# Kernel tuning notes

Hardware: AMD Instinct MI355X
Metric: run time of the kernel (lower is better)

The kernel has to match this reference:

```python
import jax, jax.numpy as jnp
import numpy as np

EPS = 1e-6
FEAT = 1024
HEADS = 16
HDIM = FEAT // HEADS
FF = 500


def setup_inputs() -> dict:
    key = jax.random.key(0)
    ks = jax.random.split(key, 12)
    B, S = 4, 2048
    inp = {
        "x": jax.random.normal(ks[0], (B, S, FEAT), jnp.float32),
        "mask": jax.random.randint(ks[1], (B, S, S), 0, 2, jnp.int32),
        "alpha1": jnp.ones((FEAT,), jnp.float32),
        "bias1": jnp.zeros((FEAT,), jnp.float32),
        "alpha2": jnp.ones((FEAT,), jnp.float32),
        "bias2": jnp.zeros((FEAT,), jnp.float32),
        "Wq": jax.random.normal(ks[2], (FEAT, FEAT), jnp.float32) * (1.0 / np.sqrt(FEAT)),
        "bq": jnp.zeros((FEAT,), jnp.float32),
        "Wk": jax.random.normal(ks[3], (FEAT, FEAT), jnp.float32) * (1.0 / np.sqrt(FEAT)),
        "bk": jnp.zeros((FEAT,), jnp.float32),
        "Wv": jax.random.normal(ks[4], (FEAT, FEAT), jnp.float32) * (1.0 / np.sqrt(FEAT)),
        "bv": jnp.zeros((FEAT,), jnp.float32),
        "Wo": jax.random.normal(ks[5], (FEAT, FEAT), jnp.float32) * (1.0 / np.sqrt(FEAT)),
        "bo": jnp.zeros((FEAT,), jnp.float32),
        "W1": jax.random.normal(ks[6], (FEAT, FF), jnp.float32) * (1.0 / np.sqrt(FEAT)),
        "b1": jnp.zeros((FF,), jnp.float32),
        "W2": jax.random.normal(ks[7], (FF, FEAT), jnp.float32) * (1.0 / np.sqrt(FF)),
        "b2": jnp.zeros((FEAT,), jnp.float32),
    }
    return inp


def _norm(x, alpha, bias):
    m = jnp.mean(x, axis=-1, keepdims=True)
    # torch.std uses Bessel's correction (ddof=1)
    s = jnp.std(x, axis=-1, keepdims=True, ddof=1)
    return alpha * (x - m) / (s + EPS) + bias


def _attn(x2, mask, Wq, bq, Wk, bk, Wv, bv, Wo, bo):
    B, S, _ = x2.shape
    q = (x2 @ Wq + bq).reshape(B, S, HEADS, HDIM)
    k = (x2 @ Wk + bk).reshape(B, S, HEADS, HDIM)
    v = (x2 @ Wv + bv).reshape(B, S, HEADS, HDIM)
    scores = jnp.einsum("bqhd,bkhd->bhqk", q, k) / np.sqrt(HDIM).astype(np.float32)
    # faithful to source: masked positions filled with -1e-09 (not -1e9)
    scores = jnp.where(mask[:, None, :, :] == 0, jnp.float32(-1e-09), scores)
    probs = jax.nn.softmax(scores, axis=-1)
    out = jnp.einsum("bhqk,bkhd->bqhd", probs, v).reshape(B, S, FEAT)
    return out @ Wo + bo


def reference(x, mask, alpha1, bias1, alpha2, bias2, Wq, bq, Wk, bk, Wv, bv, Wo, bo, W1, b1, W2, b2):
    x2 = _norm(x, alpha1, bias1)
    x = x + _attn(x2, mask, Wq, bq, Wk, bk, Wv, bv, Wo, bo)
    x2 = _norm(x, alpha2, bias2)
    h = jax.nn.elu(x2 @ W1 + b1)
    x = x + (h @ W2 + b2)
    return x
```

## Files before the change

kernel.cpp:

```cpp
#include <hip/hip_runtime.h>
#include <hip/hip_bf16.h>
#include <math.h>

#define BATCH 4
#define SEQ 2048
#define FEAT 1024
#define HEADS 16
#define HDIM 64
#define FF 500
#define FFP 512
#define ROWS (BATCH * SEQ)
#define QKVSTR 3072

typedef unsigned short ushortT;
typedef __attribute__((ext_vector_type(8))) short short8;
typedef __attribute__((ext_vector_type(4))) float floatx4;

#if defined(__has_builtin) && __has_builtin(__builtin_amdgcn_exp2f)
#define EXP2F(x) __builtin_amdgcn_exp2f(x)
#else
#define EXP2F(x) exp2f(x)
#endif

__device__ __forceinline__ unsigned short f2bf(float f) {
    unsigned int u = __builtin_bit_cast(unsigned int, f);
    u += 0x7fffu + ((u >> 16) & 1u);
    return (unsigned short)(u >> 16);
}
__device__ __forceinline__ float bf2f(short b) {
    unsigned int u = ((unsigned int)(unsigned short)b) << 16;
    return __builtin_bit_cast(float, u);
}

__device__ __forceinline__ void async16(void* lds, const void* g) {
    __builtin_amdgcn_global_load_lds(
        (const __attribute__((address_space(1))) unsigned int*)g,
        (__attribute__((address_space(3))) unsigned int*)lds, 16, 0, 0);
}

__global__ void wt_kernel(const float* __restrict__ W, ushortT* __restrict__ Wt,
                          int K, int N, int Kp)
{
    __shared__ float T[64][65];
    const int n0 = blockIdx.x * 64, k0 = blockIdx.y * 64;
    const int tid = threadIdx.x;
    const int r = tid >> 4;
    const int c = (tid & 15) * 4;
    #pragma unroll
    for (int i = 0; i < 4; i++) {
        const int kk = k0 + r + i * 16;
        #pragma unroll
        for (int e = 0; e < 4; e++) {
            const int nn = n0 + c + e;
            T[r + i * 16][c + e] = (kk < K && nn < N) ? W[(size_t)kk * N + nn] : 0.0f;
        }
    }
    __syncthreads();
    #pragma unroll
    for (int i = 0; i < 4; i++) {
        const int nn = r + i * 16;
        ushort4 o;
        o.x = f2bf(T[c + 0][nn]);
        o.y = f2bf(T[c + 1][nn]);
        o.z = f2bf(T[c + 2][nn]);
        o.w = f2bf(T[c + 3][nn]);
        *(ushort4*)(Wt + (size_t)(n0 + nn) * Kp + k0 + c) = o;
    }
}

__global__ void pad_bias_kernel(const float* __restrict__ b, float* __restrict__ bp)
{
    const int i = threadIdx.x;
    if (i < FFP) bp[i] = (i < FF) ? b[i] : 0.0f;
}

__global__ void concat_bias_kernel(const float* __restrict__ bq, const float* __restrict__ bk,
                                   const float* __restrict__ bv, float* __restrict__ o)
{
    const int i = blockIdx.x * 256 + threadIdx.x;
    o[i] = (i < 1024) ? bq[i] : ((i < 2048) ? bk[i - 1024] : bv[i - 2048]);
}

__global__ void maskbits_kernel(const int* __restrict__ mask,
                                unsigned int* __restrict__ bits)
{
    const size_t g = (size_t)blockIdx.x * 256 + threadIdx.x;
    const int lane = threadIdx.x & 63;
    const unsigned long long bal = __ballot(mask[g] != 0);
    if (lane == 0)  bits[g >> 5] = (unsigned int)bal;
    if (lane == 32) bits[g >> 5] = (unsigned int)(bal >> 32);
}

__global__ void ln_kernel(const float* __restrict__ x,
                          const float* __restrict__ alpha,
                          const float* __restrict__ bias,
                          ushortT* __restrict__ out)
{
    __shared__ float red[256];
    const int row = blockIdx.x;
    const int tid = threadIdx.x;
    float4 v = ((const float4*)(x + (size_t)row * FEAT))[tid];

    red[tid] = v.x + v.y + v.z + v.w; __syncthreads();
    for (int off = 128; off > 0; off >>= 1) {
        if (tid < off) red[tid] += red[tid + off];
        __syncthreads();
    }
    const float mean = red[0] * (1.0f / 1024.0f);
    __syncthreads();

    const float dx = v.x - mean, dy = v.y - mean, dz = v.z - mean, dw = v.w - mean;
    red[tid] = dx*dx + dy*dy + dz*dz + dw*dw; __syncthreads();
    for (int off = 128; off > 0; off >>= 1) {
        if (tid < off) red[tid] += red[tid + off];
        __syncthreads();
    }
    const float var = red[0] * (1.0f / 1023.0f);
    const float inv = 1.0f / (sqrtf(var) + 1e-6f);

    const float4 a = ((const float4*)alpha)[tid];
    const float4 b = ((const float4*)bias)[tid];
    ushort4 o;
    o.x = f2bf(a.x * dx * inv + b.x);
    o.y = f2bf(a.y * dy * inv + b.y);
    o.z = f2bf(a.z * dz * inv + b.z);
    o.w = f2bf(a.w * dw * inv + b.w);
    ((ushort4*)(out + (size_t)row * FEAT))[tid] = o;
}

template<int ACT, int RES, int OUT_BF16, int BN>
__global__ __launch_bounds__(256)
void mfma_gemm(const ushortT* __restrict__ A, const ushortT* __restrict__ Bt,
               const float* __restrict__ bias, const float* __restrict__ R,
               void* __restrict__ Cout, int M, int N, int K)
{
    constexpr int MT = (BN == 128) ? 4 : 2;
    constexpr int MSPAN = (BN == 128) ? 64 : 32;
    __shared__ ushortT As[128 * 32];
    __shared__ ushortT Bs[BN * 32];

    const int tid  = threadIdx.x;
    const int wave = tid >> 6, lane = tid & 63;
    const int quad = lane >> 4, l16 = lane & 15;
    const int wm = (BN == 128) ? (wave >> 1) : wave;
    const int wn = (BN == 128) ? (wave & 1) : 0;
    const int row0 = blockIdx.y * 128, col0 = blockIdx.x * BN;

    const floatx4 z4 = {0.f, 0.f, 0.f, 0.f};
    floatx4 acc[MT][4];
    #pragma unroll
    for (int i = 0; i < MT; i++)
        #pragma unroll
        for (int j = 0; j < 4; j++) acc[i][j] = z4;

    for (int k0 = 0; k0 < K; k0 += 32) {
        __syncthreads();
        #pragma unroll
        for (int i = 0; i < 2; i++) {
            const int rbase = 16 * (wave + 4 * i);
            const int r = rbase + (lane >> 2);
            const int co = (lane & 3) * 8;
            async16((char*)As + rbase * 64, A + (size_t)(row0 + r) * K + k0 + co);
        }
        if (BN == 128) {
            #pragma unroll
            for (int i = 0; i < 2; i++) {
                const int rbase = 16 * (wave + 4 * i);
                const int r = rbase + (lane >> 2);
                const int co = (lane & 3) * 8;
                async16((char*)Bs + rbase * 64, Bt + (size_t)(col0 + r) * K + k0 + co);
            }
        } else {
            const int rbase = 16 * wave;
            const int r = rbase + (lane >> 2);
            const int co = (lane & 3) * 8;
            async16((char*)Bs + rbase * 64, Bt + (size_t)(col0 + r) * K + k0 + co);
        }
        __syncthreads();

        short8 af[MT], bf[4];
        #pragma unroll
        for (int mt = 0; mt < MT; mt++)
            af[mt] = *(const short8*)&As[(MSPAN * wm + 16 * mt + l16) * 32 + quad * 8];
        #pragma unroll
        for (int nt = 0; nt < 4; nt++)
            bf[nt] = *(const short8*)&Bs[(64 * wn + 16 * nt + l16) * 32 + quad * 8];
        #pragma unroll
        for (int mt = 0; mt < MT; mt++)
            #pragma unroll
            for (int nt = 0; nt < 4; nt++)
                acc[mt][nt] = __builtin_amdgcn_mfma_f32_16x16x32_bf16(
                    af[mt], bf[nt], acc[mt][nt], 0, 0, 0);
    }

    #pragma unroll
    for (int mt = 0; mt < MT; mt++) {
        #pragma unroll
        for (int nt = 0; nt < 4; nt++) {
            const int col = col0 + 64 * wn + 16 * nt + l16;
            #pragma unroll
            for (int r = 0; r < 4; r++) {
                const int row = row0 + MSPAN * wm + 16 * mt + quad * 4 + r;
                float val = acc[mt][nt][r] + bias[col];
                if (ACT == 1) val = (val > 0.0f) ? val : (__expf(val) - 1.0f);
                if (RES) val += R[(size_t)row * N + col];
                if (OUT_BF16)
                    ((ushortT*)Cout)[(size_t)row * N + col] = f2bf(val);
                else
                    ((float*)Cout)[(size_t)row * N + col] = val;
            }
        }
    }
}

__global__ void transpose_v_kernel(const ushortT* __restrict__ v, ushortT* __restrict__ vt)
{
    __shared__ ushortT T[64][80];
    const int bid = blockIdx.x;
    const int jt = bid & 31, h = (bid >> 5) & 15, b = bid >> 9;
    const int j0 = jt * 64;
    const int tid = threadIdx.x;

    const int j = tid >> 2;
    #pragma unroll
    for (int i = 0; i < 2; i++) {
        const int c = (tid & 3) * 2 + i;
        short8 val = *(const short8*)(v + (size_t)(b * SEQ + j0 + j) * QKVSTR + h * 64 + c * 8);
        *(short8*)&T[j][c * 8] = val;
    }
    __syncthreads();
    const int d = tid >> 2;
    #pragma unroll
    for (int i = 0; i < 2; i++) {
        const int cj = (tid & 3) * 2 + i;
        union { short8 v8; ushortT u[8]; } tmp;
        #pragma unroll
        for (int e = 0; e < 8; e++) tmp.u[e] = T[cj * 8 + e][d];
        *(short8*)(vt + ((size_t)((b * HEADS + h) * 64 + d)) * SEQ + j0 + cj * 8) = tmp.v8;
    }
}

__global__ __launch_bounds__(256)
void mfma_attn(const ushortT* __restrict__ qkv, const ushortT* __restrict__ vt,
               const unsigned int* __restrict__ mbits, ushortT* __restrict__ attn_out)
{
    __shared__ ushortT Ks[2][64 * 64];
    __shared__ ushortT Vts[2][64 * 64];
    __shared__ ushortT Ps[64 * 64];

    const int tid = threadIdx.x;
    const int wave = tid >> 6, lane = tid & 63;
    const int quad = lane >> 4, l16 = lane & 15;
    const int bid = blockIdx.x;
    const int qt = bid & 31, h = (bid >> 5) & 15, b = bid >> 9;
    const int q0 = qt * 64;

    const ushortT* qptr = qkv;
    const ushortT* kptr = qkv + 1024;

    const size_t qrow = (size_t)(b * SEQ + q0 + wave * 16 + l16);
    short8 qf[2];
    {
        short8 t0 = *(const short8*)(qptr + qrow * QKVSTR + h * 64 + quad * 8);
        short8 t1 = *(const short8*)(qptr + qrow * QKVSTR + h * 64 + 32 + quad * 8);
        const float cs = 0.125f * 1.4426950408889634f;
        #pragma unroll
        for (int i = 0; i < 8; i++) {
            qf[0][i] = (short)f2bf(bf2f(t0[i]) * cs);
            qf[1][i] = (short)f2bf(bf2f(t1[i]) * cs);
        }
    }

    short8 ones8;
    #pragma unroll
    for (int i = 0; i < 8; i++) ones8[i] = (short)0x3F80;

    const floatx4 z4 = {0.f, 0.f, 0.f, 0.f};
    floatx4 o[4];
    #pragma unroll
    for (int dt = 0; dt < 4; dt++) o[dt] = z4;
    floatx4 lacc = z4;

    const int rr = tid >> 2;
    const int c0 = (tid & 3) * 2;
    const size_t kbase = (size_t)(b * SEQ) * QKVSTR + h * 64;
    const size_t vtbase = ((size_t)((b * HEADS + h) * 64 + rr)) * SEQ;
    short8 rk0, rk1, rv0, rv1;

#define ATTN_ISSUE(J0) {                                                     \
    const ushortT* gk = kptr + kbase + (size_t)((J0) + rr) * QKVSTR;         \
    const ushortT* gv = vt + vtbase + (J0);                                  \
    rk0 = *(const short8*)(gk + c0 * 8);                                     \
    rk1 = *(const short8*)(gk + c0 * 8 + 8);                                 \
    rv0 = *(const short8*)(gv + c0 * 8);                                     \
    rv1 = *(const short8*)(gv + c0 * 8 + 8); }

#define ATTN_WRITE(BI) {                                                     \
    *(short8*)&Ks[BI][rr * 64 + ((c0 ^ (rr & 7)) * 8)] = rk0;                \
    *(short8*)&Ks[BI][rr * 64 + (((c0 + 1) ^ (rr & 7)) * 8)] = rk1;          \
    *(short8*)&Vts[BI][rr * 64 + ((c0 ^ (rr & 7)) * 8)] = rv0;               \
    *(short8*)&Vts[BI][rr * 64 + (((c0 + 1) ^ (rr & 7)) * 8)] = rv1; }

    const int mloc = wave * 16 + l16;
    const unsigned int* mrow = mbits + (size_t)(b * SEQ + q0 + mloc) * (SEQ / 32);

    ATTN_ISSUE(0);
    ATTN_WRITE(0);

    for (int jt = 0; jt < 32; jt++) {
        __syncthreads();
        const int cur = jt & 1;
        const unsigned int w0 = mrow[jt * 2];
        const unsigned int w1 = mrow[jt * 2 + 1];
        if (jt < 31) ATTN_ISSUE((jt + 1) * 64);

        floatx4 st[4];
        #pragma unroll
        for (int nt = 0; nt < 4; nt++) {
            const int j = nt * 16 + l16;
            short8 ka0 = *(const short8*)&Ks[cur][j * 64 + ((quad ^ (j & 7)) * 8)];
            short8 ka1 = *(const short8*)&Ks[cur][j * 64 + (((4 + quad) ^ (j & 7)) * 8)];
            floatx4 t = z4;
            t = __builtin_amdgcn_mfma_f32_16x16x32_bf16(ka0, qf[0], t, 0, 0, 0);
            t = __builtin_amdgcn_mfma_f32_16x16x32_bf16(ka1, qf[1], t, 0, 0, 0);
            st[nt] = t;
        }

        #pragma unroll
        for (int nt = 0; nt < 4; nt++) {
            const unsigned int w = (nt & 2) ? w1 : w0;
            const unsigned int wsh = w >> ((nt & 1) * 16 + quad * 4);
            float p[4];
            p[0] = EXP2F((wsh & 1u) ? st[nt][0] : 0.0f);
            p[1] = EXP2F((wsh & 2u) ? st[nt][1] : 0.0f);
            p[2] = EXP2F((wsh & 4u) ? st[nt][2] : 0.0f);
            p[3] = EXP2F((wsh & 8u) ? st[nt][3] : 0.0f);
            const int j0 = nt * 16 + quad * 4;
            const int chunk = (j0 >> 3) ^ (mloc & 7);
            const int ci = j0 & 7;
            ushortT* dst = &Ps[mloc * 64 + chunk * 8 + ci];
            *(__hip_bfloat162*)(dst)     = __float22bfloat162_rn(make_float2(p[0], p[1]));
            *(__hip_bfloat162*)(dst + 2) = __float22bfloat162_rn(make_float2(p[2], p[3]));
        }

        {
            short8 pa0 = *(const short8*)&Ps[mloc * 64 + ((quad ^ (mloc & 7)) * 8)];
            short8 pa1 = *(const short8*)&Ps[mloc * 64 + (((4 + quad) ^ (mloc & 7)) * 8)];
            lacc = __builtin_amdgcn_mfma_f32_16x16x32_bf16(pa0, ones8, lacc, 0, 0, 0);
            lacc = __builtin_amdgcn_mfma_f32_16x16x32_bf16(pa1, ones8, lacc, 0, 0, 0);
            #pragma unroll
            for (int dt = 0; dt < 4; dt++) {
                const int d = dt * 16 + l16;
                short8 vb0 = *(const short8*)&Vts[cur][d * 64 + ((quad ^ (d & 7)) * 8)];
                short8 vb1 = *(const short8*)&Vts[cur][d * 64 + (((4 + quad) ^ (d & 7)) * 8)];
                o[dt] = __builtin_amdgcn_mfma_f32_16x16x32_bf16(pa0, vb0, o[dt], 0, 0, 0);
                o[dt] = __builtin_amdgcn_mfma_f32_16x16x32_bf16(pa1, vb1, o[dt], 0, 0, 0);
            }
        }

        if (jt < 31) ATTN_WRITE((jt + 1) & 1);
    }

    #pragma unroll
    for (int r = 0; r < 4; r++) {
        const float inv_l = 1.0f / lacc[r];
        const size_t row = (size_t)(b * SEQ + q0 + wave * 16 + quad * 4 + r);
        #pragma unroll
        for (int dt = 0; dt < 4; dt++) {
            attn_out[row * FEAT + h * 64 + dt * 16 + l16] = f2bf(o[dt][r] * inv_l);
        }
    }
#undef ATTN_ISSUE
#undef ATTN_WRITE
}

extern "C" void kernel_launch(void* const* d_in, const int* in_sizes, int n_in,
                              void* d_out, int out_size, void* d_ws, size_t ws_size,
                              hipStream_t stream)
{
    const float* x      = (const float*)d_in[0];
    const int*   mask   = (const int*)d_in[1];
    const float* alpha1 = (const float*)d_in[2];
    const float* bias1  = (const float*)d_in[3];
    const float* alpha2 = (const float*)d_in[4];
    const float* bias2  = (const float*)d_in[5];
    const float* Wq     = (const float*)d_in[6];
    const float* bq     = (const float*)d_in[7];
    const float* Wk     = (const float*)d_in[8];
    const float* bk     = (const float*)d_in[9];
    const float* Wv     = (const float*)d_in[10];
    const float* bv     = (const float*)d_in[11];
    const float* Wo     = (const float*)d_in[12];
    const float* bo     = (const float*)d_in[13];
    const float* W1     = (const float*)d_in[14];
    const float* b1     = (const float*)d_in[15];
    const float* W2     = (const float*)d_in[16];
    const float* b2     = (const float*)d_in[17];
    float* out = (float*)d_out;

    char* ws = (char*)d_ws;
    const size_t MB = 1024 * 1024;
    ushortT* x2b    = (ushortT*)(ws);
    ushortT* attn_o = (ushortT*)(ws);
    ushortT* qkv    = (ushortT*)(ws + 16 * MB);
    ushortT* x2b2   = (ushortT*)(ws + 16 * MB);
    ushortT* hbuf   = (ushortT*)(ws + 32 * MB);
    ushortT* vtb    = (ushortT*)(ws + 64 * MB);
    ushortT* Wqkvt  = (ushortT*)(ws + 80 * MB);
    ushortT* Wot    = (ushortT*)(ws + 86 * MB);
    ushortT* W1t    = (ushortT*)(ws + 88 * MB);
    ushortT* W2t    = (ushortT*)(ws + 89 * MB);
    float*   b1p    = (float*)  (ws + 90 * MB);
    float*   bqkv   = (float*)  (ws + 90 * MB + 16384);
    unsigned int* mbits = (unsigned int*)(ws + 91 * MB);

    const dim3 blk(256);

    wt_kernel<<<dim3(16, 16), blk, 0, stream>>>(Wq, Wqkvt,                  FEAT, FEAT, FEAT);
    wt_kernel<<<dim3(16, 16), blk, 0, stream>>>(Wk, Wqkvt + 1024 * FEAT,    FEAT, FEAT, FEAT);
    wt_kernel<<<dim3(16, 16), blk, 0, stream>>>(Wv, Wqkvt + 2048 * FEAT,    FEAT, FEAT, FEAT);
    wt_kernel<<<dim3(16, 16), blk, 0, stream>>>(Wo, Wot, FEAT, FEAT, FEAT);
    wt_kernel<<<dim3(8, 16),  blk, 0, stream>>>(W1, W1t, FEAT, FF, FEAT);
    wt_kernel<<<dim3(16, 8),  blk, 0, stream>>>(W2, W2t, FF, FEAT, FFP);
    pad_bias_kernel<<<1, FFP, 0, stream>>>(b1, b1p);
    concat_bias_kernel<<<12, blk, 0, stream>>>(bq, bk, bv, bqkv);
    maskbits_kernel<<<(BATCH * SEQ * SEQ) / 256, blk, 0, stream>>>(mask, mbits);

    ln_kernel<<<ROWS, blk, 0, stream>>>(x, alpha1, bias1, x2b);

    mfma_gemm<0, 0, 1, 128><<<dim3(24, 64), blk, 0, stream>>>(
        x2b, Wqkvt, bqkv, nullptr, qkv, ROWS, QKVSTR, FEAT);

    transpose_v_kernel<<<BATCH * HEADS * (SEQ / 64), blk, 0, stream>>>(qkv + 2048, vtb);
    mfma_attn<<<BATCH * HEADS * (SEQ / 64), blk, 0, stream>>>(qkv, vtb, mbits, attn_o);

    mfma_gemm<0, 1, 0, 128><<<dim3(8, 64), blk, 0, stream>>>(
        attn_o, Wot, bo, x, out, ROWS, FEAT, FEAT);

    ln_kernel<<<ROWS, blk, 0, stream>>>(out, alpha2, bias2, x2b2);

    mfma_gemm<1, 0, 1, 64><<<dim3(FFP / 64, 64), blk, 0, stream>>>(
        x2b2, W1t, b1p, nullptr, hbuf, ROWS, FFP, FEAT);

    mfma_gemm<0, 1, 0, 128><<<dim3(8, 64), blk, 0, stream>>>(
        hbuf, W2t, b2, out, out, ROWS, FEAT, FFP);
}
```

Measured before the change: 516.7 us.

## Enlarge attention query tile, deepen GEMM K-step, fuse prep kernels, shuffle LayerNorm

Attention blocks now cover 128 query rows, with two 16-row groups per wave. Each K/V tile loaded into LDS is therefore reused twice, which halves K/V global traffic and the number of blocks. The GEMM now stages a 64-wide K slice in two LDS buffers per iteration, halving the barrier count at the cost of twice the LDS. The weight-transpose and bias kernels are merged into one launch, and LayerNorm uses wave shuffles with single-pass sum/sum-of-squares instead of a tree reduction. The single-pass variance is slightly less numerically robust, and attention register pressure rises.

```diff
diff --git a/kernel.cpp b/kernel.cpp
--- a/kernel.cpp
+++ b/kernel.cpp
@@ -11,6 +11,7 @@
 #define FFP 512
 #define ROWS (BATCH * SEQ)
 #define QKVSTR 3072
+#define AQ 128
 
 typedef unsigned short ushortT;
 typedef __attribute__((ext_vector_type(8))) short short8;
@@ -38,12 +39,40 @@
         (__attribute__((address_space(3))) unsigned int*)lds, 16, 0, 0);
 }
 
-__global__ void wt_kernel(const float* __restrict__ W, ushortT* __restrict__ Wt,
-                          int K, int N, int Kp)
-{
+__global__ void prep_kernel(const float* __restrict__ Wq, const float* __restrict__ Wk,
+                            const float* __restrict__ Wv, const float* __restrict__ Wo,
+                            const float* __restrict__ W1, const float* __restrict__ W2,
+                            const float* __restrict__ bq, const float* __restrict__ bk,
+                            const float* __restrict__ bv, const float* __restrict__ b1,
+                            ushortT* __restrict__ Wqkvt, ushortT* __restrict__ Wot,
+                            ushortT* __restrict__ W1t, ushortT* __restrict__ W2t,
+                            float* __restrict__ bqkv, float* __restrict__ b1p)
+{
+    const int t = blockIdx.x;
+    const int tid = threadIdx.x;
+    if (t == 1280) {
+        for (int i = tid; i < QKVSTR; i += 256)
+            bqkv[i] = (i < 1024) ? bq[i] : ((i < 2048) ? bk[i - 1024] : bv[i - 2048]);
+        for (int i = tid; i < FFP; i += 256)
+            b1p[i] = (i < FF) ? b1[i] : 0.0f;
+        return;
+    }
+    const float* W; ushortT* Wt; int K, N, Kp, bx, by;
+    if (t < 1024) {
+        const int wi = t >> 8, lt = t & 255;
+        bx = lt & 15; by = lt >> 4; K = FEAT; N = FEAT; Kp = FEAT;
+        W  = (wi == 0) ? Wq : (wi == 1) ? Wk : (wi == 2) ? Wv : Wo;
+        Wt = (wi == 3) ? Wot : (Wqkvt + (size_t)wi * FEAT * FEAT);
+    } else if (t < 1152) {
+        const int lt = t - 1024; bx = lt & 7; by = lt >> 3;
+        K = FEAT; N = FF; Kp = FEAT; W = W1; Wt = W1t;
+    } else {
+        const int lt = t - 1152; bx = lt & 15; by = lt >> 4;
+        K = FF; N = FEAT; Kp = FFP; W = W2; Wt = W2t;
+    }
+
     __shared__ float T[64][65];
-    const int n0 = blockIdx.x * 64, k0 = blockIdx.y * 64;
-    const int tid = threadIdx.x;
+    const int n0 = bx * 64, k0 = by * 64;
     const int r = tid >> 4;
     const int c = (tid & 15) * 4;
     #pragma unroll
@@ -59,6 +88,7 @@
     #pragma unroll
     for (int i = 0; i < 4; i++) {
         const int nn = r + i * 16;
+        if (n0 + nn >= N && Kp == FEAT && N == FF) continue;
         ushort4 o;
         o.x = f2bf(T[c + 0][nn]);
         o.y = f2bf(T[c + 1][nn]);
@@ -68,19 +98,6 @@
     }
 }
 
-__global__ void pad_bias_kernel(const float* __restrict__ b, float* __restrict__ bp)
-{
-    const int i = threadIdx.x;
-    if (i < FFP) bp[i] = (i < FF) ? b[i] : 0.0f;
-}
-
-__global__ void concat_bias_kernel(const float* __restrict__ bq, const float* __restrict__ bk,
-                                   const float* __restrict__ bv, float* __restrict__ o)
-{
-    const int i = blockIdx.x * 256 + threadIdx.x;
-    o[i] = (i < 1024) ? bq[i] : ((i < 2048) ? bk[i - 1024] : bv[i - 2048]);
-}
-
 __global__ void maskbits_kernel(const int* __restrict__ mask,
                                 unsigned int* __restrict__ bits)
 {
@@ -96,35 +113,34 @@
                           const float* __restrict__ bias,
                           ushortT* __restrict__ out)
 {
-    __shared__ float red[256];
+    __shared__ float p1[4], p2[4];
     const int row = blockIdx.x;
     const int tid = threadIdx.x;
+    const int wave = tid >> 6, lane = tid & 63;
     float4 v = ((const float4*)(x + (size_t)row * FEAT))[tid];
 
-    red[tid] = v.x + v.y + v.z + v.w; __syncthreads();
-    for (int off = 128; off > 0; off >>= 1) {
-        if (tid < off) red[tid] += red[tid + off];
-        __syncthreads();
-    }
-    const float mean = red[0] * (1.0f / 1024.0f);
+    float s1 = v.x + v.y + v.z + v.w;
+    float s2 = v.x * v.x + v.y * v.y + v.z * v.z + v.w * v.w;
+    #pragma unroll
+    for (int off = 32; off > 0; off >>= 1) {
+        s1 += __shfl_xor(s1, off);
+        s2 += __shfl_xor(s2, off);
+    }
+    if (lane == 0) { p1[wave] = s1; p2[wave] = s2; }
     __syncthreads();
-
-    const float dx = v.x - mean, dy = v.y - mean, dz = v.z - mean, dw = v.w - mean;
-    red[tid] = dx*dx + dy*dy + dz*dz + dw*dw; __syncthreads();
-    for (int off = 128; off > 0; off >>= 1) {
-        if (tid < off) red[tid] += red[tid + off];
-        __syncthreads();
-    }
-    const float var = red[0] * (1.0f / 1023.0f);
+    const float t1 = p1[0] + p1[1] + p1[2] + p1[3];
+    const float t2 = p2[0] + p2[1] + p2[2] + p2[3];
+    const float mean = t1 * (1.0f / 1024.0f);
+    const float var = fmaxf(t2 - 1024.0f * mean * mean, 0.0f) * (1.0f / 1023.0f);
     const float inv = 1.0f / (sqrtf(var) + 1e-6f);
 
     const float4 a = ((const float4*)alpha)[tid];
     const float4 b = ((const float4*)bias)[tid];
     ushort4 o;
-    o.x = f2bf(a.x * dx * inv + b.x);
-    o.y = f2bf(a.y * dy * inv + b.y);
-    o.z = f2bf(a.z * dz * inv + b.z);
-    o.w = f2bf(a.w * dw * inv + b.w);
+    o.x = f2bf(a.x * (v.x - mean) * inv + b.x);
+    o.y = f2bf(a.y * (v.y - mean) * inv + b.y);
+    o.z = f2bf(a.z * (v.z - mean) * inv + b.z);
+    o.w = f2bf(a.w * (v.w - mean) * inv + b.w);
     ((ushort4*)(out + (size_t)row * FEAT))[tid] = o;
 }
 
@@ -136,8 +152,8 @@
 {
     constexpr int MT = (BN == 128) ? 4 : 2;
     constexpr int MSPAN = (BN == 128) ? 64 : 32;
-    __shared__ ushortT As[128 * 32];
-    __shared__ ushortT Bs[BN * 32];
+    __shared__ ushortT As[2][128 * 32];
+    __shared__ ushortT Bs[2][BN * 32];
 
     const int tid  = threadIdx.x;
     const int wave = tid >> 6, lane = tid & 63;
@@ -153,44 +169,53 @@
         #pragma unroll
         for (int j = 0; j < 4; j++) acc[i][j] = z4;
 
-    for (int k0 = 0; k0 < K; k0 += 32) {
+    for (int k0 = 0; k0 < K; k0 += 64) {
         __syncthreads();
         #pragma unroll
-        for (int i = 0; i < 2; i++) {
-            const int rbase = 16 * (wave + 4 * i);
-            const int r = rbase + (lane >> 2);
-            const int co = (lane & 3) * 8;
-            async16((char*)As + rbase * 64, A + (size_t)(row0 + r) * K + k0 + co);
-        }
-        if (BN == 128) {
+        for (int kh = 0; kh < 2; kh++) {
             #pragma unroll
             for (int i = 0; i < 2; i++) {
                 const int rbase = 16 * (wave + 4 * i);
                 const int r = rbase + (lane >> 2);
                 const int co = (lane & 3) * 8;
-                async16((char*)Bs + rbase * 64, Bt + (size_t)(col0 + r) * K + k0 + co);
-            }
-        } else {
-            const int rbase = 16 * wave;
-            const int r = rbase + (lane >> 2);
-            const int co = (lane & 3) * 8;
-            async16((char*)Bs + rbase * 64, Bt + (size_t)(col0 + r) * K + k0 + co);
+                async16((char*)As[kh] + rbase * 64,
+                        A + (size_t)(row0 + r) * K + k0 + kh * 32 + co);
+            }
+            if (BN == 128) {
+                #pragma unroll
+                for (int i = 0; i < 2; i++) {
+                    const int rbase = 16 * (wave + 4 * i);
+                    const int r = rbase + (lane >> 2);
+                    const int co = (lane & 3) * 8;
+                    async16((char*)Bs[kh] + rbase * 64,
+                            Bt + (size_t)(col0 + r) * K + k0 + kh * 32 + co);
+                }
+            } else {
+                const int rbase = 16 * wave;
+                const int r = rbase + (lane >> 2);
+                const int co = (lane & 3) * 8;
+                async16((char*)Bs[kh] + rbase * 64,
+                        Bt + (size_t)(col0 + r) * K + k0 + kh * 32 + co);
+            }
         }
         __syncthreads();
 
-        short8 af[MT], bf[4];
-        #pragma unroll
-        for (int mt = 0; mt < MT; mt++)
-            af[mt] = *(const short8*)&As[(MSPAN * wm + 16 * mt + l16) * 32 + quad * 8];
-        #pragma unroll
-        for (int nt = 0; nt < 4; nt++)
-            bf[nt] = *(const short8*)&Bs[(64 * wn + 16 * nt + l16) * 32 + quad * 8];
-        #pragma unroll
-        for (int mt = 0; mt < MT; mt++)
+        #pragma unroll
+        for (int kh = 0; kh < 2; kh++) {
+            short8 af[MT], bf[4];
+            #pragma unroll
+            for (int mt = 0; mt < MT; mt++)
+                af[mt] = *(const short8*)&As[kh][(MSPAN * wm + 16 * mt + l16) * 32 + quad * 8];
             #pragma unroll
             for (int nt = 0; nt < 4; nt++)
-                acc[mt][nt] = __builtin_amdgcn_mfma_f32_16x16x32_bf16(
-                    af[mt], bf[nt], acc[mt][nt], 0, 0, 0);
+                bf[nt] = *(const short8*)&Bs[kh][(64 * wn + 16 * nt + l16) * 32 + quad * 8];
+            #pragma unroll
+            for (int mt = 0; mt < MT; mt++)
+                #pragma unroll
+                for (int nt = 0; nt < 4; nt++)
+                    acc[mt][nt] = __builtin_amdgcn_mfma_f32_16x16x32_bf16(
+                        af[mt], bf[nt], acc[mt][nt], 0, 0, 0);
+        }
     }
 
     #pragma unroll
@@ -246,28 +271,29 @@
 {
     __shared__ ushortT Ks[2][64 * 64];
     __shared__ ushortT Vts[2][64 * 64];
-    __shared__ ushortT Ps[64 * 64];
+    __shared__ ushortT Ps[AQ * 64];
 
     const int tid = threadIdx.x;
     const int wave = tid >> 6, lane = tid & 63;
     const int quad = lane >> 4, l16 = lane & 15;
     const int bid = blockIdx.x;
-    const int qt = bid & 31, h = (bid >> 5) & 15, b = bid >> 9;
-    const int q0 = qt * 64;
+    const int qt = bid & 15, h = (bid >> 4) & 15, b = bid >> 8;
+    const int q0 = qt * AQ;
 
     const ushortT* qptr = qkv;
     const ushortT* kptr = qkv + 1024;
 
-    const size_t qrow = (size_t)(b * SEQ + q0 + wave * 16 + l16);
-    short8 qf[2];
-    {
+    short8 qf[2][2];
+    #pragma unroll
+    for (int mg = 0; mg < 2; mg++) {
+        const size_t qrow = (size_t)(b * SEQ + q0 + 32 * wave + mg * 16 + l16);
         short8 t0 = *(const short8*)(qptr + qrow * QKVSTR + h * 64 + quad * 8);
         short8 t1 = *(const short8*)(qptr + qrow * QKVSTR + h * 64 + 32 + quad * 8);
         const float cs = 0.125f * 1.4426950408889634f;
         #pragma unroll
         for (int i = 0; i < 8; i++) {
-            qf[0][i] = (short)f2bf(bf2f(t0[i]) * cs);
-            qf[1][i] = (short)f2bf(bf2f(t1[i]) * cs);
+            qf[mg][0][i] = (short)f2bf(bf2f(t0[i]) * cs);
+            qf[mg][1][i] = (short)f2bf(bf2f(t1[i]) * cs);
         }
     }
 
@@ -276,24 +302,25 @@
     for (int i = 0; i < 8; i++) ones8[i] = (short)0x3F80;
 
     const floatx4 z4 = {0.f, 0.f, 0.f, 0.f};
-    floatx4 o[4];
-    #pragma unroll
-    for (int dt = 0; dt < 4; dt++) o[dt] = z4;
-    floatx4 lacc = z4;
+    floatx4 o[2][4];
+    #pragma unroll
+    for (int mg = 0; mg < 2; mg++)
+        #pragma unroll
+        for (int dt = 0; dt < 4; dt++) o[mg][dt] = z4;
+    floatx4 lacc[2] = {z4, z4};
 
     const int rr = tid >> 2;
     const int c0 = (tid & 3) * 2;
-    const size_t kbase = (size_t)(b * SEQ) * QKVSTR + h * 64;
-    const size_t vtbase = ((size_t)((b * HEADS + h) * 64 + rr)) * SEQ;
+    const ushortT* gk = kptr + (size_t)(b * SEQ + rr) * QKVSTR + h * 64;
+    const ushortT* gv = vt + ((size_t)((b * HEADS + h) * 64 + rr)) * SEQ;
     short8 rk0, rk1, rv0, rv1;
 
-#define ATTN_ISSUE(J0) {                                                     \
-    const ushortT* gk = kptr + kbase + (size_t)((J0) + rr) * QKVSTR;         \
-    const ushortT* gv = vt + vtbase + (J0);                                  \
+#define ATTN_ISSUE() {                                                       \
     rk0 = *(const short8*)(gk + c0 * 8);                                     \
     rk1 = *(const short8*)(gk + c0 * 8 + 8);                                 \
     rv0 = *(const short8*)(gv + c0 * 8);                                     \
-    rv1 = *(const short8*)(gv + c0 * 8 + 8); }
+    rv1 = *(const short8*)(gv + c0 * 8 + 8);                                 \
+    gk += (size_t)64 * QKVSTR; gv += 64; }
 
 #define ATTN_WRITE(BI) {                                                     \
     *(short8*)&Ks[BI][rr * 64 + ((c0 ^ (rr & 7)) * 8)] = rk0;                \
@@ -301,73 +328,96 @@
     *(short8*)&Vts[BI][rr * 64 + ((c0 ^ (rr & 7)) * 8)] = rv0;               \
     *(short8*)&Vts[BI][rr * 64 + (((c0 + 1) ^ (rr & 7)) * 8)] = rv1; }
 
-    const int mloc = wave * 16 + l16;
-    const unsigned int* mrow = mbits + (size_t)(b * SEQ + q0 + mloc) * (SEQ / 32);
-
-    ATTN_ISSUE(0);
+    const unsigned int* mrowp[2];
+    mrowp[0] = mbits + (size_t)(b * SEQ + q0 + 32 * wave + l16) * (SEQ / 32);
+    mrowp[1] = mrowp[0] + 16 * (SEQ / 32);
+    const int mloc0 = 32 * wave + l16;
+
+    ATTN_ISSUE();
     ATTN_WRITE(0);
 
+    #pragma unroll 2
     for (int jt = 0; jt < 32; jt++) {
         __syncthreads();
         const int cur = jt & 1;
-        const unsigned int w0 = mrow[jt * 2];
-        const unsigned int w1 = mrow[jt * 2 + 1];
-        if (jt < 31) ATTN_ISSUE((jt + 1) * 64);
-
-        floatx4 st[4];
+        unsigned int w[2][2];
+        #pragma unroll
+        for (int mg = 0; mg < 2; mg++) {
+            w[mg][0] = mrowp[mg][jt * 2];
+            w[mg][1] = mrowp[mg][jt * 2 + 1];
+        }
+        if (jt < 31) ATTN_ISSUE();
+
+        floatx4 st[2][4];
         #pragma unroll
         for (int nt = 0; nt < 4; nt++) {
             const int j = nt * 16 + l16;
             short8 ka0 = *(const short8*)&Ks[cur][j * 64 + ((quad ^ (j & 7)) * 8)];
             short8 ka1 = *(const short8*)&Ks[cur][j * 64 + (((4 + quad) ^ (j & 7)) * 8)];
-            floatx4 t = z4;
-            t = __builtin_amdgcn_mfma_f32_16x16x32_bf16(ka0, qf[0], t, 0, 0, 0);
-            t = __builtin_amdgcn_mfma_f32_16x16x32_bf16(ka1, qf[1], t, 0, 0, 0);
-            st[nt] = t;
-        }
-
-        #pragma unroll
-        for (int nt = 0; nt < 4; nt++) {
-            const unsigned int w = (nt & 2) ? w1 : w0;
-            const unsigned int wsh = w >> ((nt & 1) * 16 + quad * 4);
-            float p[4];
-            p[0] = EXP2F((wsh & 1u) ? st[nt][0] : 0.0f);
-            p[1] = EXP2F((wsh & 2u) ? st[nt][1] : 0.0f);
-            p[2] = EXP2F((wsh & 4u) ? st[nt][2] : 0.0f);
-            p[3] = EXP2F((wsh & 8u) ? st[nt][3] : 0.0f);
-            const int j0 = nt * 16 + quad * 4;
-            const int chunk = (j0 >> 3) ^ (mloc & 7);
-            const int ci = j0 & 7;
-            ushortT* dst = &Ps[mloc * 64 + chunk * 8 + ci];
-            *(__hip_bfloat162*)(dst)     = __float22bfloat162_rn(make_float2(p[0], p[1]));
-            *(__hip_bfloat162*)(dst + 2) = __float22bfloat162_rn(make_float2(p[2], p[3]));
-        }
-
-        {
-            short8 pa0 = *(const short8*)&Ps[mloc * 64 + ((quad ^ (mloc & 7)) * 8)];
-            short8 pa1 = *(const short8*)&Ps[mloc * 64 + (((4 + quad) ^ (mloc & 7)) * 8)];
-            lacc = __builtin_amdgcn_mfma_f32_16x16x32_bf16(pa0, ones8, lacc, 0, 0, 0);
-            lacc = __builtin_amdgcn_mfma_f32_16x16x32_bf16(pa1, ones8, lacc, 0, 0, 0);
+            #pragma unroll
+            for (int mg = 0; mg < 2; mg++) {
+                floatx4 t = z4;
+                t = __builtin_amdgcn_mfma_f32_16x16x32_bf16(ka0, qf[mg][0], t, 0, 0, 0);
+                t = __builtin_amdgcn_mfma_f32_16x16x32_bf16(ka1, qf[mg][1], t, 0, 0, 0);
+                st[mg][nt] = t;
+            }
+        }
+
+        #pragma unroll
+        for (int mg = 0; mg < 2; mg++) {
+            const int mloc = mloc0 + mg * 16;
+            #pragma unroll
+            for (int nt = 0; nt < 4; nt++) {
+                const unsigned int ww = (nt & 2) ? w[mg][1] : w[mg][0];
+                const unsigned int wsh = ww >> ((nt & 1) * 16 + quad * 4);
+                float p[4];
+                p[0] = EXP2F((wsh & 1u) ? st[mg][nt][0] : 0.0f);
+                p[1] = EXP2F((wsh & 2u) ? st[mg][nt][1] : 0.0f);
+                p[2] = EXP2F((wsh & 4u) ? st[mg][nt][2] : 0.0f);
+                p[3] = EXP2F((wsh & 8u) ? st[mg][nt][3] : 0.0f);
+                const int j0 = nt * 16 + quad * 4;
+                const int chunk = (j0 >> 3) ^ (mloc & 7);
+                const int ci = j0 & 7;
+                ushortT* dst = &Ps[mloc * 64 + chunk * 8 + ci];
+                *(__hip_bfloat162*)(dst)     = __float22bfloat162_rn(make_float2(p[0], p[1]));
+                *(__hip_bfloat162*)(dst + 2) = __float22bfloat162_rn(make_float2(p[2], p[3]));
+            }
+        }
+
+        short8 pa[2][2];
+        #pragma unroll
+        for (int mg = 0; mg < 2; mg++) {
+            const int mloc = mloc0 + mg * 16;
+            pa[mg][0] = *(const short8*)&Ps[mloc * 64 + ((quad ^ (mloc & 7)) * 8)];
+            pa[mg][1] = *(const short8*)&Ps[mloc * 64 + (((4 + quad) ^ (mloc & 7)) * 8)];
+            lacc[mg] = __builtin_amdgcn_mfma_f32_16x16x32_bf16(pa[mg][0], ones8, lacc[mg], 0, 0, 0);
+            lacc[mg] = __builtin_amdgcn_mfma_f32_16x16x32_bf16(pa[mg][1], ones8, lacc[mg], 0, 0, 0);
+        }
+        #pragma unroll
+        for (int dt = 0; dt < 4; dt++) {
+            const int d = dt * 16 + l16;
+            short8 vb0 = *(const short8*)&Vts[cur][d * 64 + ((quad ^ (d & 7)) * 8)];
+            short8 vb1 = *(const short8*)&Vts[cur][d * 64 + (((4 + quad) ^ (d & 7)) * 8)];
+            #pragma unroll
+            for (int mg = 0; mg < 2; mg++) {
+                o[mg][dt] = __builtin_amdgcn_mfma_f32_16x16x32_bf16(pa[mg][0], vb0, o[mg][dt], 0, 0, 0);
+                o[mg][dt] = __builtin_amdgcn_mfma_f32_16x16x32_bf16(pa[mg][1], vb1, o[mg][dt], 0, 0, 0);
+            }
+        }
+
+        if (jt < 31) ATTN_WRITE(cur ^ 1);
+    }
+
+    #pragma unroll
+    for (int mg = 0; mg < 2; mg++) {
+        #pragma unroll
+        for (int r = 0; r < 4; r++) {
+            const float inv_l = 1.0f / lacc[mg][r];
+            const size_t row = (size_t)(b * SEQ + q0 + 32 * wave + mg * 16 + quad * 4 + r);
             #pragma unroll
             for (int dt = 0; dt < 4; dt++) {
-                const int d = dt * 16 + l16;
-                short8 vb0 = *(const short8*)&Vts[cur][d * 64 + ((quad ^ (d & 7)) * 8)];
-                short8 vb1 = *(const short8*)&Vts[cur][d * 64 + (((4 + quad) ^ (d & 7)) * 8)];
-                o[dt] = __builtin_amdgcn_mfma_f32_16x16x32_bf16(pa0, vb0, o[dt], 0, 0, 0);
-                o[dt] = __builtin_amdgcn_mfma_f32_16x16x32_bf16(pa1, vb1, o[dt], 0, 0, 0);
-            }
-        }
-
-        if (jt < 31) ATTN_WRITE((jt + 1) & 1);
-    }
-
-    #pragma unroll
-    for (int r = 0; r < 4; r++) {
-        const float inv_l = 1.0f / lacc[r];
-        const size_t row = (size_t)(b * SEQ + q0 + wave * 16 + quad * 4 + r);
-        #pragma unroll
-        for (int dt = 0; dt < 4; dt++) {
-            attn_out[row * FEAT + h * 64 + dt * 16 + l16] = f2bf(o[dt][r] * inv_l);
+                attn_out[row * FEAT + h * 64 + dt * 16 + l16] = f2bf(o[mg][dt][r] * inv_l);
+            }
         }
     }
 #undef ATTN_ISSUE
@@ -416,14 +466,8 @@
 
     const dim3 blk(256);
 
-    wt_kernel<<<dim3(16, 16), blk, 0, stream>>>(Wq, Wqkvt,                  FEAT, FEAT, FEAT);
-    wt_kernel<<<dim3(16, 16), blk, 0, stream>>>(Wk, Wqkvt + 1024 * FEAT,    FEAT, FEAT, FEAT);
-    wt_kernel<<<dim3(16, 16), blk, 0, stream>>>(Wv, Wqkvt + 2048 * FEAT,    FEAT, FEAT, FEAT);
-    wt_kernel<<<dim3(16, 16), blk, 0, stream>>>(Wo, Wot, FEAT, FEAT, FEAT);
-    wt_kernel<<<dim3(8, 16),  blk, 0, stream>>>(W1, W1t, FEAT, FF, FEAT);
-    wt_kernel<<<dim3(16, 8),  blk, 0, stream>>>(W2, W2t, FF, FEAT, FFP);
-    pad_bias_kernel<<<1, FFP, 0, stream>>>(b1, b1p);
-    concat_bias_kernel<<<12, blk, 0, stream>>>(bq, bk, bv, bqkv);
+    prep_kernel<<<1281, blk, 0, stream>>>(Wq, Wk, Wv, Wo, W1, W2, bq, bk, bv, b1,
+                                          Wqkvt, Wot, W1t, W2t, bqkv, b1p);
     maskbits_kernel<<<(BATCH * SEQ * SEQ) / 256, blk, 0, stream>>>(mask, mbits);
 
     ln_kernel<<<ROWS, blk, 0, stream>>>(x, alpha1, bias1, x2b);
@@ -432,7 +476,7 @@
         x2b, Wqkvt, bqkv, nullptr, qkv, ROWS, QKVSTR, FEAT);
 
     transpose_v_kernel<<<BATCH * HEADS * (SEQ / 64), blk, 0, stream>>>(qkv + 2048, vtb);
-    mfma_attn<<<BATCH * HEADS * (SEQ / 64), blk, 0, stream>>>(qkv, vtb, mbits, attn_o);
+    mfma_attn<<<BATCH * HEADS * (SEQ / AQ), blk, 0, stream>>>(qkv, vtb, mbits, attn_o);
 
     mfma_gemm<0, 1, 0, 128><<<dim3(8, 64), blk, 0, stream>>>(
         attn_o, Wot, bo, x, out, ROWS, FEAT, FEAT);
```

New measurement: 473.4 us. 8.4% less time.
